# Kernel optimization log

Hardware: AMD Instinct MI355X
Metric: run time of the kernel (lower is better)

Reference implementation:

```python
import jax, jax.numpy as jnp
import numpy as np

D_MODEL = 256; N_HEADS = 8; N_LEVELS = 4; N_POINTS = 4; D_FFN = 1024
SHAPES = [(128, 128), (64, 64), (32, 32), (16, 16)]  # (H, W) per level, strides 8/16/32/64 of 1024x1024 input
B = 8; LQ = 1024
S_TOT = sum(h * w for h, w in SHAPES)


def setup_inputs() -> dict:
    key = jax.random.key(0)
    ks = iter(jax.random.split(key, 48))
    d = D_MODEL

    def f(shape, s=0.02):
        return jax.random.normal(next(ks), shape, dtype=jnp.float32) * s

    return {
        'tgt': f((B, LQ, d), 1.0),
        'query_pos': f((B, LQ, d), 1.0),
        'reference_points': jax.random.uniform(next(ks), (B, LQ, N_LEVELS, 2), dtype=jnp.float32),
        'src': f((B, S_TOT, d), 1.0),
        'w_in': f((3 * d, d)), 'b_in': jnp.zeros((3 * d,), jnp.float32),
        'w_out': f((d, d)), 'b_out': jnp.zeros((d,), jnp.float32),
        'ln1_g': jnp.ones((d,), jnp.float32), 'ln1_b': jnp.zeros((d,), jnp.float32),
        'ln2_g': jnp.ones((d,), jnp.float32), 'ln2_b': jnp.zeros((d,), jnp.float32),
        'ln3_g': jnp.ones((d,), jnp.float32), 'ln3_b': jnp.zeros((d,), jnp.float32),
        'w_val': f((d, d)), 'b_val': jnp.zeros((d,), jnp.float32),
        'w_off': f((N_HEADS * N_LEVELS * N_POINTS * 2, d), 0.002),
        'b_off': f((N_HEADS * N_LEVELS * N_POINTS * 2,), 0.5),
        'w_attw': f((N_HEADS * N_LEVELS * N_POINTS, d)),
        'b_attw': jnp.zeros((N_HEADS * N_LEVELS * N_POINTS,), jnp.float32),
        'w_oc': f((d, d)), 'b_oc': jnp.zeros((d,), jnp.float32),
        'w1': f((D_FFN, d)), 'b1': jnp.zeros((D_FFN,), jnp.float32),
        'w2': f((d, D_FFN)), 'b2': jnp.zeros((d,), jnp.float32),
        'spatial_shapes': jnp.array(SHAPES, dtype=jnp.int32),
    }


def layer_norm(x, g, b):
    mu = x.mean(-1, keepdims=True)
    var = ((x - mu) ** 2).mean(-1, keepdims=True)
    return (x - mu) * jax.lax.rsqrt(var + 1e-5) * g + b


def mha(tgt, query_pos, w_in, b_in, w_out, b_out):
    d = D_MODEL; Dh = d // N_HEADS
    Bs, Lq, _ = tgt.shape
    qk = tgt + query_pos
    q = (qk @ w_in[:d].T + b_in[:d]).reshape(Bs, Lq, N_HEADS, Dh)
    k = (qk @ w_in[d:2 * d].T + b_in[d:2 * d]).reshape(Bs, Lq, N_HEADS, Dh)
    v = (tgt @ w_in[2 * d:].T + b_in[2 * d:]).reshape(Bs, Lq, N_HEADS, Dh)
    attn = jax.nn.softmax(jnp.einsum('bqhd,bkhd->bhqk', q, k) / np.sqrt(Dh).astype(np.float32), axis=-1)
    o = jnp.einsum('bhqk,bkhd->bqhd', attn, v).reshape(Bs, Lq, d)
    return o @ w_out.T + b_out


def ms_deform_attn(value, loc, attw):
    # value [B,S,H,Dh]; loc [B,Lq,H,L,P,2] in [0,1]; attw [B,Lq,H,L,P]
    Bs, _, Hh, Dh = value.shape
    Lq = loc.shape[1]

    def to_hfirst(x):  # [B,Lq,Hh,P] -> [B,Hh,Lq*P,1]
        return jnp.transpose(x, (0, 2, 1, 3)).reshape(Bs, Hh, Lq * N_POINTS, 1)

    acc = jnp.zeros((Bs, Hh, Lq * N_POINTS, Dh), value.dtype)
    start = 0
    for l, (H_, W_) in enumerate(SHAPES):
        v = jnp.transpose(value[:, start:start + H_ * W_], (0, 2, 1, 3))  # [B,Hh,HW,Dh]
        start += H_ * W_
        ll = loc[:, :, :, l]  # [B,Lq,Hh,P,2]
        x = ll[..., 0] * W_ - 0.5
        y = ll[..., 1] * H_ - 0.5
        x0 = jnp.floor(x); y0 = jnp.floor(y)
        tx = x - x0; ty = y - y0

        def gather(xi, yi):
            valid = ((xi >= 0) & (xi < W_) & (yi >= 0) & (yi < H_)).astype(value.dtype)
            fi = (jnp.clip(yi, 0, H_ - 1) * W_ + jnp.clip(xi, 0, W_ - 1)).astype(jnp.int32)
            g = jnp.take_along_axis(v, to_hfirst(fi.astype(jnp.float32)).astype(jnp.int32), axis=2)
            return g * to_hfirst(valid)

        samp = (gather(x0, y0) * to_hfirst((1 - tx) * (1 - ty))
                + gather(x0 + 1, y0) * to_hfirst(tx * (1 - ty))
                + gather(x0, y0 + 1) * to_hfirst((1 - tx) * ty)
                + gather(x0 + 1, y0 + 1) * to_hfirst(tx * ty))
        acc = acc + samp * to_hfirst(attw[:, :, :, l])
    out = acc.reshape(Bs, Hh, Lq, N_POINTS, Dh).sum(3)  # [B,Hh,Lq,Dh]
    return jnp.transpose(out, (0, 2, 1, 3)).reshape(Bs, Lq, Hh * Dh)


def reference(tgt, query_pos, reference_points, src, w_in, b_in, w_out, b_out,
              ln1_g, ln1_b, ln2_g, ln2_b, ln3_g, ln3_b,
              w_val, b_val, w_off, b_off, w_attw, b_attw, w_oc, b_oc,
              w1, b1, w2, b2, spatial_shapes):
    Bs, Lq, d = tgt.shape
    Dh = d // N_HEADS
    # --- self attention (q=k=tgt+pos, v=tgt), residual + norm2 ---
    t2 = mha(tgt, query_pos, w_in, b_in, w_out, b_out)
    tgt = layer_norm(tgt + t2, ln2_g, ln2_b)
    # --- MSDeformAttn cross attention, residual + norm1 ---
    query = tgt + query_pos
    value = (src @ w_val.T + b_val).reshape(Bs, -1, N_HEADS, Dh)
    off = (query @ w_off.T + b_off).reshape(Bs, Lq, N_HEADS, N_LEVELS, N_POINTS, 2)
    aw = jax.nn.softmax((query @ w_attw.T + b_attw).reshape(Bs, Lq, N_HEADS, N_LEVELS * N_POINTS), axis=-1)
    aw = aw.reshape(Bs, Lq, N_HEADS, N_LEVELS, N_POINTS)
    normalizer = jnp.array([[w, h] for h, w in SHAPES], dtype=tgt.dtype)  # (W,H) per level
    loc = reference_points[:, :, None, :, None, :] + off / normalizer[None, None, None, :, None, :]
    ca = ms_deform_attn(value, loc, aw) @ w_oc.T + b_oc
    tgt = layer_norm(tgt + ca, ln1_g, ln1_b)
    # --- FFN, residual + norm3 ---
    t2 = jax.nn.relu(tgt @ w1.T + b1) @ w2.T + b2
    tgt = layer_norm(tgt + t2, ln3_g, ln3_b)
    return tgt
```

## Files before the change

### kernel.cpp

```cpp
#include <hip/hip_runtime.h>

typedef unsigned short ushort_t;
typedef unsigned int uint_t;
typedef __attribute__((ext_vector_type(8))) short short8;
typedef __attribute__((ext_vector_type(4))) float floatx4;
typedef __attribute__((ext_vector_type(4))) unsigned short ushortx4;

__device__ __forceinline__ ushort_t f2bf(float f){
  uint_t u = __builtin_bit_cast(uint_t, f);
  u += 0x7FFFu + ((u >> 16) & 1u);
  return (ushort_t)(u >> 16);
}
__device__ __forceinline__ float bf2f(ushort_t u){
  uint_t x = ((uint_t)u) << 16;
  return __builtin_bit_cast(float, x);
}
__device__ __forceinline__ uint_t packbf2(float a, float b){
  return (uint_t)f2bf(a) | ((uint_t)f2bf(b) << 16);
}

__device__ __forceinline__ void gload16(const void* g, void* l){
  __builtin_amdgcn_global_load_lds(
      (const __attribute__((address_space(1))) void*)g,
      (__attribute__((address_space(3))) void*)l, 16, 0, 0);
}

__global__ __launch_bounds__(256) void convert_w_kernel(const float* __restrict__ w_in_v,
    const float* __restrict__ w_val, const float* __restrict__ w_out,
    const float* __restrict__ w_oc, const float* __restrict__ w1,
    const float* __restrict__ w2, ushort_t* __restrict__ dst){
  int j = (blockIdx.x*256 + threadIdx.x) * 4;
  if (j >= 786432) return;
  const float* src; int off;
  if      (j <  65536){ src = w_in_v; off = 0;      }
  else if (j < 131072){ src = w_val;  off = 65536;  }
  else if (j < 196608){ src = w_out;  off = 131072; }
  else if (j < 262144){ src = w_oc;   off = 196608; }
  else if (j < 524288){ src = w1;     off = 262144; }
  else                { src = w2;     off = 524288; }
  float4 v = *(const float4*)(src + (j - off));
  uint2 u; u.x = packbf2(v.x, v.y); u.y = packbf2(v.z, v.w);
  *(uint2*)(dst + j) = u;
}

__global__ __launch_bounds__(256) void addln_kernel(const float* __restrict__ X,
    const float* __restrict__ Y, const float* __restrict__ gw,
    const float* __restrict__ bw, float* __restrict__ Out){
  int wave = threadIdx.x >> 6, lane = threadIdx.x & 63;
  long row = (long)blockIdx.x * 4 + wave;
  long base = row * 256 + lane * 4;
  float4 x = *(const float4*)(X + base);
  float4 y = *(const float4*)(Y + base);
  float v0=x.x+y.x, v1=x.y+y.y, v2=x.z+y.z, v3=x.w+y.w;
  float s  = v0+v1+v2+v3;
  float sq = v0*v0+v1*v1+v2*v2+v3*v3;
  #pragma unroll
  for (int off=32; off>0; off>>=1){
    s  += __shfl_xor(s, off);
    sq += __shfl_xor(sq, off);
  }
  float mu  = s * (1.f/256.f);
  float var = sq * (1.f/256.f) - mu*mu;
  float rs  = rsqrtf(var + 1e-5f);
  float4 g4 = *(const float4*)(gw + lane*4);
  float4 b4 = *(const float4*)(bw + lane*4);
  float4 o;
  o.x = (v0-mu)*rs*g4.x + b4.x;
  o.y = (v1-mu)*rs*g4.y + b4.y;
  o.z = (v2-mu)*rs*g4.z + b4.z;
  o.w = (v3-mu)*rs*g4.w + b4.w;
  *(float4*)(Out + base) = o;
}

__device__ __forceinline__ void stage_store(ushort_t* ls, int r, int c4, float4 v){
  int byte = r*64 + ((((c4>>1) ^ ((r>>1)&3)) << 4) | ((c4&1) << 3));
  uint2 u; u.x = packbf2(v.x, v.y); u.y = packbf2(v.z, v.w);
  *(uint2*)((char*)ls + byte) = u;
}
__device__ __forceinline__ short8 frag_load(const ushort_t* ls, int r, int g){
  int byte = r*64 + ((g ^ ((r>>1)&3)) << 4);
  return *(const short8*)((const char*)ls + byte);
}

__device__ __forceinline__ short8 frag_load_f32(const float* ls, int r, int g){
  const char* base = (const char*)ls + r*128;
  int x = r & 7;
  float4 f0 = *(const float4*)(base + ((((2*g)  ^ x)) << 4));
  float4 f1 = *(const float4*)(base + ((((2*g+1)^ x)) << 4));
  uint4 u;
  u.x = packbf2(f0.x, f0.y); u.y = packbf2(f0.z, f0.w);
  u.z = packbf2(f1.x, f1.y); u.w = packbf2(f1.z, f1.w);
  return __builtin_bit_cast(short8, u);
}

template<bool RELU, bool OUT_BF16>
__global__ __launch_bounds__(256) void gemm_dma_kernel(const float* __restrict__ A,
    const ushort_t* __restrict__ Wbf, const float* __restrict__ bias,
    void* __restrict__ Cout, int M, int N, int K){
  __shared__ float    ldsA[2][4096];
  __shared__ ushort_t ldsB[2][4096];
  const int t = threadIdx.x;
  const int lane = t & 63, wave = t >> 6;
  const int wm = wave >> 1, wn = wave & 1;
  const long rowA0 = (long)blockIdx.x * 128;
  const long rowB0 = (long)blockIdx.y * 128;
  const int rr = lane & 15, g = lane >> 4;
  const int arow  = lane >> 3;
  const int aslot = (lane & 7) ^ (arow & 7);
  const float* Abase = A + (rowA0 + wave*32 + arow)*(long)K + aslot*4;
  const int brow  = lane >> 2;
  const int bslot = lane & 3;
  floatx4 acc[4][4] = {};
  const int nsteps = K >> 5;

  #define ISSUE(kk, buf) do { \
    _Pragma("unroll") \
    for (int c=0;c<4;++c) \
      gload16(Abase + (kk) + (long)(8*c)*K, &ldsA[buf][(wave*32 + 8*c)*32]); \
    _Pragma("unroll") \
    for (int c=0;c<2;++c){ \
      int r_ = wave*32 + c*16 + brow; \
      const ushort_t* bs_ = Wbf + (rowB0 + r_)*(long)K + (kk) + (bslot ^ ((r_>>1)&3))*8; \
      gload16(bs_, (char*)ldsB[buf] + (wave*32 + c*16)*64); \
    } \
  } while(0)

  ISSUE(0, 0);
  if (nsteps > 1) ISSUE(32, 1);

  for (int k = 0; k < nsteps; ++k){
    if (k < nsteps-1) asm volatile("s_waitcnt vmcnt(6)" ::: "memory");
    else              asm volatile("s_waitcnt vmcnt(0)" ::: "memory");
    __builtin_amdgcn_s_barrier();
    const float*    lA = ldsA[k & 1];
    const ushort_t* lB = ldsB[k & 1];
    short8 af[4], bfr[4];
    #pragma unroll
    for (int mi=0;mi<4;++mi) af[mi]  = frag_load_f32(lA, wm*64 + mi*16 + rr, g);
    #pragma unroll
    for (int ni=0;ni<4;++ni) bfr[ni] = frag_load(lB, wn*64 + ni*16 + rr, g);
    #pragma unroll
    for (int mi=0;mi<4;++mi)
      #pragma unroll
      for (int ni=0;ni<4;++ni)
        acc[mi][ni] = __builtin_amdgcn_mfma_f32_16x16x32_bf16(af[mi], bfr[ni], acc[mi][ni], 0, 0, 0);
    __builtin_amdgcn_s_barrier();
    if (k + 2 < nsteps) ISSUE((k+2)*32, k & 1);
  }
  #undef ISSUE

  const int cg = lane >> 4;
  #pragma unroll
  for (int ni=0;ni<4;++ni){
    long n = rowB0 + wn*64 + ni*16 + (lane & 15);
    float bv = bias[n];
    #pragma unroll
    for (int mi=0;mi<4;++mi){
      long m = rowA0 + wm*64 + mi*16 + cg*4;
      #pragma unroll
      for (int r2=0;r2<4;++r2){
        float v = acc[mi][ni][r2] + bv;
        if (RELU) v = fmaxf(v, 0.f);
        if (OUT_BF16) ((ushort_t*)Cout)[(m+r2)*N + n] = f2bf(v);
        else          ((float*)Cout)[(m+r2)*N + n] = v;
      }
    }
  }
}

template<bool RELU, bool OUT_BF16>
__global__ __launch_bounds__(512, 4) void gemm_dma2_kernel(const float* __restrict__ A,
    const ushort_t* __restrict__ Wbf, const float* __restrict__ bias,
    void* __restrict__ Cout, int M, int N, int K){
  __shared__ float    ldsA[2][4096];
  __shared__ ushort_t ldsB[2][8192];
  const int t = threadIdx.x;
  const int lane = t & 63, wave = t >> 6;
  const int wm = wave >> 2, wn = wave & 3;
  const long rowA0 = (long)blockIdx.x * 128;
  const long n0 = (long)blockIdx.y * 256;
  const int rr = lane & 15, g = lane >> 4;
  const int arow_in = lane >> 3;
  const int aslot   = (lane & 7) ^ (arow_in & 7);
  const int brow_in = lane >> 2;
  const int bslot   = lane & 3;
  floatx4 acc[4][4] = {};
  const int nsteps = K >> 5;

  #define ISSUE2(kk, buf) do { \
    _Pragma("unroll") \
    for (int c=0;c<2;++c){ \
      int ar_ = (wave*2 + c)*8 + arow_in; \
      gload16(A + (rowA0 + ar_)*(long)K + (kk) + aslot*4, \
              &ldsA[buf][(wave*2 + c)*8*32]); \
    } \
    _Pragma("unroll") \
    for (int c=0;c<2;++c){ \
      int br_ = (wave*2 + c)*16 + brow_in; \
      const ushort_t* bs_ = Wbf + (n0 + br_)*(long)K + (kk) + (bslot ^ ((br_>>1)&3))*8; \
      gload16(bs_, (char*)ldsB[buf] + (wave*2 + c)*16*64); \
    } \
  } while(0)

  ISSUE2(0, 0);
  if (nsteps > 1) ISSUE2(32, 1);

  for (int k = 0; k < nsteps; ++k){
    if (k < nsteps-1) asm volatile("s_waitcnt vmcnt(4)" ::: "memory");
    else              asm volatile("s_waitcnt vmcnt(0)" ::: "memory");
    __builtin_amdgcn_s_barrier();
    const float*    lA = ldsA[k & 1];
    const ushort_t* lB = ldsB[k & 1];
    short8 af[4], bfr[4];
    #pragma unroll
    for (int mi=0;mi<4;++mi) af[mi]  = frag_load_f32(lA, wm*64 + mi*16 + rr, g);
    #pragma unroll
    for (int ni=0;ni<4;++ni) bfr[ni] = frag_load(lB, wn*64 + ni*16 + rr, g);
    #pragma unroll
    for (int mi=0;mi<4;++mi)
      #pragma unroll
      for (int ni=0;ni<4;++ni)
        acc[mi][ni] = __builtin_amdgcn_mfma_f32_16x16x32_bf16(af[mi], bfr[ni], acc[mi][ni], 0, 0, 0);
    __builtin_amdgcn_s_barrier();
    if (k + 2 < nsteps) ISSUE2((k+2)*32, k & 1);
  }
  #undef ISSUE2

  const int cg = lane >> 4;
  #pragma unroll
  for (int ni=0;ni<4;++ni){
    long n = n0 + wn*64 + ni*16 + (lane & 15);
    float bv = bias[n];
    #pragma unroll
    for (int mi=0;mi<4;++mi){
      long m = rowA0 + wm*64 + mi*16 + cg*4;
      #pragma unroll
      for (int r2=0;r2<4;++r2){
        float v = acc[mi][ni][r2] + bv;
        if (RELU) v = fmaxf(v, 0.f);
        if (OUT_BF16) ((ushort_t*)Cout)[(m+r2)*N + n] = f2bf(v);
        else          ((float*)Cout)[(m+r2)*N + n] = v;
      }
    }
  }
}

template<bool RELU>
__global__ __launch_bounds__(256) void gemm_add2_kernel(const float* __restrict__ A,
    const float* __restrict__ A2, const float* __restrict__ W,
    const float* __restrict__ bias, void* __restrict__ Cout,
    int M, int N, int K){
  __shared__ ushort_t lsA[4096], lsB[4096];
  const int t = threadIdx.x;
  const int lane = t & 63, wave = t >> 6;
  const int wm = wave >> 1, wn = wave & 1;
  const long rowA0 = (long)blockIdx.x * 128;
  const long rowB0 = (long)blockIdx.y * 128;
  floatx4 acc[4][4] = {};
  const int rr = lane & 15, g = lane >> 4;
  const int rA = t >> 3, c4 = t & 7;
  const float* Ap = A + (rowA0 + rA)*(long)K + c4*4;
  const float* A2p = A2 + (rowA0 + rA)*(long)K + c4*4;
  const float* Wp = W + (rowB0 + rA)*(long)K + c4*4;

  for (int k0 = 0; k0 < K; k0 += 32){
    __syncthreads();
    #pragma unroll
    for (int j=0;j<4;++j){
      float4 v = *(const float4*)(Ap + k0 + (long)(32*j)*K);
      float4 y = *(const float4*)(A2p + k0 + (long)(32*j)*K);
      v.x+=y.x; v.y+=y.y; v.z+=y.z; v.w+=y.w;
      stage_store(lsA, rA + 32*j, c4, v);
      stage_store(lsB, rA + 32*j, c4, *(const float4*)(Wp + k0 + (long)(32*j)*K));
    }
    __syncthreads();
    short8 af[4], bfr[4];
    #pragma unroll
    for (int mi=0;mi<4;++mi) af[mi]  = frag_load(lsA, wm*64 + mi*16 + rr, g);
    #pragma unroll
    for (int ni=0;ni<4;++ni) bfr[ni] = frag_load(lsB, wn*64 + ni*16 + rr, g);
    #pragma unroll
    for (int mi=0;mi<4;++mi)
      #pragma unroll
      for (int ni=0;ni<4;++ni)
        acc[mi][ni] = __builtin_amdgcn_mfma_f32_16x16x32_bf16(af[mi], bfr[ni], acc[mi][ni], 0, 0, 0);
  }
  const int cg = lane >> 4;
  #pragma unroll
  for (int ni=0;ni<4;++ni){
    long n = rowB0 + wn*64 + ni*16 + (lane & 15);
    float bv = bias[n];
    #pragma unroll
    for (int mi=0;mi<4;++mi){
      long m = rowA0 + wm*64 + mi*16 + cg*4;
      #pragma unroll
      for (int r2=0;r2<4;++r2){
        float v = acc[mi][ni][r2] + bv;
        if (RELU) v = fmaxf(v, 0.f);
        ((float*)Cout)[(m+r2)*N + n] = v;
      }
    }
  }
}

__global__ __launch_bounds__(256) void attn_mfma_kernel(const float* __restrict__ QK,
    const float* __restrict__ V, float* __restrict__ O){
  __shared__ ushort_t lsQ[4096];
  __shared__ ushort_t lsK[1024];
  __shared__ ushort_t lsVT[1024];
  __shared__ ushort_t lsP[4096];
  const int bh = blockIdx.y, b = bh >> 3, h = bh & 7;
  const int qt0 = blockIdx.x * 128;
  const int t = threadIdx.x, lane = t & 63, w = t >> 6;
  const int rr = lane & 15, g = lane >> 4;
  const float csc = 0.25506332f;

  const float* qbase = QK + ((long)b*1024 + qt0)*512 + h*32;
  #pragma unroll
  for (int j=0;j<4;++j){
    int i = t + j*256; int r = i>>3, c4i = i&7;
    float4 v = *(const float4*)(qbase + (long)r*512 + c4i*4);
    stage_store(lsQ, r, c4i, v);
  }
  __syncthreads();
  short8 bq[2];
  bq[0] = frag_load(lsQ, w*32 + rr, g);
  bq[1] = frag_load(lsQ, w*32 + 16 + rr, g);

  floatx4 accO[2][2] = {};
  float rsum[2] = {0.f, 0.f};
  const float* kbase = QK + (long)b*1024*512 + 256 + h*32;
  const float* vbase = V  + (long)b*1024*256 + h*32;

  for (int kt = 0; kt < 1024; kt += 32){
    __syncthreads();
    {
      int r = t >> 3, c4i = t & 7;
      float4 v = *(const float4*)(kbase + (long)(kt + r)*512 + c4i*4);
      stage_store(lsK, r, c4i, v);
    }
    {
      int kk = t >> 3, d4 = t & 7;
      float4 vv = *(const float4*)(vbase + (long)(kt + kk)*256 + d4*4);
      float vals[4] = {vv.x, vv.y, vv.z, vv.w};
      #pragma unroll
      for (int j=0;j<4;++j){
        int d = d4*4 + j;
        int cb = kk*2;
        int byte = d*64 + ((((cb>>4) ^ ((d>>1)&3)) << 4) | (cb & 15));
        *(ushort_t*)((char*)lsVT + byte) = f2bf(vals[j]);
      }
    }
    __syncthreads();
    floatx4 accS[2][2] = {};
    short8 ak0 = frag_load(lsK, rr, g);
    short8 ak1 = frag_load(lsK, 16 + rr, g);
    accS[0][0] = __builtin_amdgcn_mfma_f32_16x16x32_bf16(ak0, bq[0], accS[0][0], 0,0,0);
    accS[0][1] = __builtin_amdgcn_mfma_f32_16x16x32_bf16(ak0, bq[1], accS[0][1], 0,0,0);
    accS[1][0] = __builtin_amdgcn_mfma_f32_16x16x32_bf16(ak1, bq[0], accS[1][0], 0,0,0);
    accS[1][1] = __builtin_amdgcn_mfma_f32_16x16x32_bf16(ak1, bq[1], accS[1][1], 0,0,0);
    #pragma unroll
    for (int mi=0;mi<2;++mi){
      #pragma unroll
      for (int ni=0;ni<2;++ni){
        float p0 = exp2f(accS[mi][ni][0]*csc);
        float p1 = exp2f(accS[mi][ni][1]*csc);
        float p2 = exp2f(accS[mi][ni][2]*csc);
        float p3 = exp2f(accS[mi][ni][3]*csc);
        rsum[ni] += (p0+p1)+(p2+p3);
        int q   = w*32 + ni*16 + rr;
        int k0b = (mi*16 + g*4)*2;
        int byte = q*64 + ((((k0b>>4) ^ ((q>>1)&3)) << 4) | (k0b & 15));
        uint2 u; u.x = packbf2(p0,p1); u.y = packbf2(p2,p3);
        *(uint2*)((char*)lsP + byte) = u;
      }
    }
    short8 av0 = frag_load(lsVT, rr, g);
    short8 av1 = frag_load(lsVT, 16 + rr, g);
    short8 bp0 = frag_load(lsP, w*32 + rr, g);
    short8 bp1 = frag_load(lsP, w*32 + 16 + rr, g);
    accO[0][0] = __builtin_amdgcn_mfma_f32_16x16x32_bf16(av0, bp0, accO[0][0], 0,0,0);
    accO[0][1] = __builtin_amdgcn_mfma_f32_16x16x32_bf16(av0, bp1, accO[0][1], 0,0,0);
    accO[1][0] = __builtin_amdgcn_mfma_f32_16x16x32_bf16(av1, bp0, accO[1][0], 0,0,0);
    accO[1][1] = __builtin_amdgcn_mfma_f32_16x16x32_bf16(av1, bp1, accO[1][1], 0,0,0);
  }
  #pragma unroll
  for (int ni=0;ni<2;++ni){
    rsum[ni] += __shfl_xor(rsum[ni], 16);
    rsum[ni] += __shfl_xor(rsum[ni], 32);
    float inv = 1.f / rsum[ni];
    int q = qt0 + w*32 + ni*16 + rr;
    float* op = O + ((long)b*1024 + q)*256 + h*32;
    #pragma unroll
    for (int mi=0;mi<2;++mi){
      #pragma unroll
      for (int r2=0;r2<4;++r2){
        int d = mi*16 + g*4 + r2;
        op[d] = accO[mi][ni][r2] * inv;
      }
    }
  }
}

__global__ __launch_bounds__(256) void deform_kernel(const ushort_t* __restrict__ val,
    const float* __restrict__ offs, const float* __restrict__ awl,
    const float* __restrict__ refp, float* __restrict__ Out){
  __shared__ float s_off[1024], s_aw[512], s_ref[32];
  const int t = threadIdx.x;
  const long q0 = (long)blockIdx.x * 4;
  *(float4*)(s_off + t*4) = *(const float4*)(offs + q0*256 + t*4);
  if (t < 128) *(float4*)(s_aw + t*4) = *(const float4*)(awl + q0*128 + t*4);
  if (t < 32)  s_ref[t] = refp[q0*8 + t];
  __syncthreads();
  const int qi = t >> 6, tl = t & 63;
  const int h = tl >> 3, dq = (tl & 7) << 2;
  const int bq = (int)q0 + qi;
  const int b = bq >> 10;
  const float* offp = s_off + qi*256 + h*32;
  const float* awp  = s_aw  + qi*128 + h*16;
  const float* refq = s_ref + qi*8;
  float mx = -1e30f;
  #pragma unroll
  for (int i=0;i<16;++i) mx = fmaxf(mx, awp[i]);
  float p[16], sum = 0.f;
  #pragma unroll
  for (int i=0;i<16;++i){ p[i] = expf(awp[i]-mx); sum += p[i]; }
  float inv = 1.f/sum;
  const long vb = (long)b*21760*256 + h*32 + dq;
  const int Dim[4] = {128,64,32,16};
  const int St[4]  = {0,16384,20480,21504};
  float a0=0.f, a1=0.f, a2=0.f, a3=0.f;
  #pragma unroll
  for (int l=0;l<4;++l){
    const int Wl = Dim[l], Hl = Dim[l], st = St[l];
    float rx = refq[2*l], ry = refq[2*l+1];
    #pragma unroll
    for (int pp=0;pp<4;++pp){
      float x = rx*(float)Wl + offp[l*8+pp*2]   - 0.5f;
      float y = ry*(float)Hl + offp[l*8+pp*2+1] - 0.5f;
      float xf = floorf(x), yf = floorf(y);
      int x0 = (int)xf, y0 = (int)yf;
      float tx = x - xf, ty = y - yf;
      float s0=0.f,s1=0.f,s2=0.f,s3=0.f;
      #define CORNER(XI, YI, WGT) \
        if ((XI) >= 0 && (XI) < Wl && (YI) >= 0 && (YI) < Hl){ \
          ushortx4 u = *(const ushortx4*)(val + vb + (long)(st + (YI)*Wl + (XI))*256); \
          float wq = (WGT); \
          s0 += wq*bf2f(u[0]); s1 += wq*bf2f(u[1]); \
          s2 += wq*bf2f(u[2]); s3 += wq*bf2f(u[3]); \
        }
      CORNER(x0,   y0,   (1.f-tx)*(1.f-ty));
      CORNER(x0+1, y0,   tx*(1.f-ty));
      CORNER(x0,   y0+1, (1.f-tx)*ty);
      CORNER(x0+1, y0+1, tx*ty);
      #undef CORNER
      float pw = p[l*4+pp];
      a0 += pw*s0; a1 += pw*s1; a2 += pw*s2; a3 += pw*s3;
    }
  }
  float4 o; o.x=a0*inv; o.y=a1*inv; o.z=a2*inv; o.w=a3*inv;
  *(float4*)(Out + (long)bq*256 + h*32 + dq) = o;
}

extern "C" void kernel_launch(void* const* d_in, const int* in_sizes, int n_in,
                              void* d_out, int out_size, void* d_ws, size_t ws_size,
                              hipStream_t stream){
  (void)in_sizes; (void)n_in; (void)out_size; (void)ws_size;
  const float* tgt   = (const float*)d_in[0];
  const float* qpos  = (const float*)d_in[1];
  const float* refp  = (const float*)d_in[2];
  const float* src   = (const float*)d_in[3];
  const float* w_in  = (const float*)d_in[4];
  const float* b_in  = (const float*)d_in[5];
  const float* w_out = (const float*)d_in[6];
  const float* b_out = (const float*)d_in[7];
  const float* ln1g  = (const float*)d_in[8];
  const float* ln1b  = (const float*)d_in[9];
  const float* ln2g  = (const float*)d_in[10];
  const float* ln2b  = (const float*)d_in[11];
  const float* ln3g  = (const float*)d_in[12];
  const float* ln3b  = (const float*)d_in[13];
  const float* w_val = (const float*)d_in[14];
  const float* b_val = (const float*)d_in[15];
  const float* w_off = (const float*)d_in[16];
  const float* b_off = (const float*)d_in[17];
  const float* w_attw= (const float*)d_in[18];
  const float* b_attw= (const float*)d_in[19];
  const float* w_oc  = (const float*)d_in[20];
  const float* b_oc  = (const float*)d_in[21];
  const float* w1    = (const float*)d_in[22];
  const float* b1    = (const float*)d_in[23];
  const float* w2    = (const float*)d_in[24];
  const float* b2    = (const float*)d_in[25];

  float* ws = (float*)d_ws;
  float* bufQK  = ws + 2097152;
  float* bufOff = ws + 2097152;
  float* bufAW  = ws + 4194304;
  float* bufV   = ws + 6291456;
  float* bufO   = ws + 8388608;
  float* bufT2  = ws + 10485760;
  float* bufTg1 = ws + 12582912;
  float* bufTg2 = ws + 14680064;
  ushort_t* bufVal = (ushort_t*)(ws + 16777216);
  float* bufH   = ws + 16777216;
  ushort_t* bufWbf = (ushort_t*)(ws + 39059456);
  float* outF   = (float*)d_out;

  const ushort_t* winvbf = bufWbf;
  const ushort_t* wvalbf = bufWbf + 65536;
  const ushort_t* woutbf = bufWbf + 131072;
  const ushort_t* wocbf  = bufWbf + 196608;
  const ushort_t* w1bf   = bufWbf + 262144;
  const ushort_t* w2bf   = bufWbf + 524288;

  dim3 B256(256), B512(512);
  convert_w_kernel<<<dim3(768), B256, 0, stream>>>(w_in + 512*256, w_val, w_out, w_oc, w1, w2, bufWbf);
  gemm_add2_kernel<false><<<dim3(64,4), B256, 0, stream>>>(tgt, qpos, w_in, b_in, bufQK, 8192, 512, 256);
  gemm_dma_kernel<false,false><<<dim3(64,2), B256, 0, stream>>>(tgt, winvbf, b_in + 512, bufV, 8192, 256, 256);
  attn_mfma_kernel<<<dim3(8,64), B256, 0, stream>>>(bufQK, bufV, bufO);
  gemm_dma_kernel<false,false><<<dim3(64,2), B256, 0, stream>>>(bufO, woutbf, b_out, bufT2, 8192, 256, 256);
  addln_kernel<<<dim3(2048), B256, 0, stream>>>(tgt, bufT2, ln2g, ln2b, bufTg1);
  gemm_dma2_kernel<false,true><<<dim3(1360,1), B512, 0, stream>>>(src, wvalbf, b_val, bufVal, 174080, 256, 256);
  gemm_add2_kernel<false><<<dim3(64,2), B256, 0, stream>>>(bufTg1, qpos, w_off, b_off, bufOff, 8192, 256, 256);
  gemm_add2_kernel<false><<<dim3(64,1), B256, 0, stream>>>(bufTg1, qpos, w_attw, b_attw, bufAW, 8192, 128, 256);
  deform_kernel<<<dim3(2048), B256, 0, stream>>>(bufVal, bufOff, bufAW, refp, bufO);
  gemm_dma_kernel<false,false><<<dim3(64,2), B256, 0, stream>>>(bufO, wocbf, b_oc, bufT2, 8192, 256, 256);
  addln_kernel<<<dim3(2048), B256, 0, stream>>>(bufTg1, bufT2, ln1g, ln1b, bufTg2);
  gemm_dma2_kernel<true,false><<<dim3(64,4), B512, 0, stream>>>(bufTg2, w1bf, b1, bufH, 8192, 1024, 256);
  gemm_dma_kernel<false,false><<<dim3(64,2), B256, 0, stream>>>(bufH, w2bf, b2, bufT2, 8192, 256, 1024);
  addln_kernel<<<dim3(2048), B256, 0, stream>>>(bufTg2, bufT2, ln3g, ln3b, outF);
}
```

Baseline: 350.2 us.

## Fuse offset and attention-weight projections, branchless deform sampling, wider FFN2 GEMM

Packs w_off/w_attw and their biases into one weight matrix so a single GEMM produces both sampling offsets and attention logits, with the deform kernel reading the concatenated layout. This drops one launch and a second pass over the input activations. Bilinear corner loads become branchless: indices are clamped and out-of-range weights zeroed, which removes divergence but issues loads for corners that were previously skipped. The second FFN GEMM switches to the 512-thread dma2 kernel with one column block, which changes its tiling and occupancy.

```diff
diff --git a/kernel.cpp b/kernel.cpp
--- a/kernel.cpp
+++ b/kernel.cpp
@@ -41,6 +41,19 @@
   float4 v = *(const float4*)(src + (j - off));
   uint2 u; u.x = packbf2(v.x, v.y); u.y = packbf2(v.z, v.w);
   *(uint2*)(dst + j) = u;
+}
+
+__global__ __launch_bounds__(256) void pack_offattw_kernel(const float* __restrict__ w_off,
+    const float* __restrict__ w_attw, const float* __restrict__ b_off,
+    const float* __restrict__ b_attw, float* __restrict__ dst){
+  int j = (blockIdx.x*256 + threadIdx.x) * 4;
+  if (j >= 98688) return;
+  const float* src; int off;
+  if      (j < 65536){ src = w_off;  off = 0;     }
+  else if (j < 98304){ src = w_attw; off = 65536; }
+  else if (j < 98560){ src = b_off;  off = 98304; }
+  else               { src = b_attw; off = 98560; }
+  *(float4*)(dst + j) = *(const float4*)(src + (j - off));
 }
 
 __global__ __launch_bounds__(256) void addln_kernel(const float* __restrict__ X,
@@ -403,21 +416,22 @@
 }
 
 __global__ __launch_bounds__(256) void deform_kernel(const ushort_t* __restrict__ val,
-    const float* __restrict__ offs, const float* __restrict__ awl,
-    const float* __restrict__ refp, float* __restrict__ Out){
-  __shared__ float s_off[1024], s_aw[512], s_ref[32];
+    const float* __restrict__ offaw, const float* __restrict__ refp,
+    float* __restrict__ Out){
+  __shared__ float s_cat[1536], s_ref[32];
   const int t = threadIdx.x;
   const long q0 = (long)blockIdx.x * 4;
-  *(float4*)(s_off + t*4) = *(const float4*)(offs + q0*256 + t*4);
-  if (t < 128) *(float4*)(s_aw + t*4) = *(const float4*)(awl + q0*128 + t*4);
+  const float* srcOA = offaw + q0*384;
+  *(float4*)(s_cat + t*4) = *(const float4*)(srcOA + t*4);
+  if (t < 128) *(float4*)(s_cat + 1024 + t*4) = *(const float4*)(srcOA + 1024 + t*4);
   if (t < 32)  s_ref[t] = refp[q0*8 + t];
   __syncthreads();
   const int qi = t >> 6, tl = t & 63;
   const int h = tl >> 3, dq = (tl & 7) << 2;
   const int bq = (int)q0 + qi;
   const int b = bq >> 10;
-  const float* offp = s_off + qi*256 + h*32;
-  const float* awp  = s_aw  + qi*128 + h*16;
+  const float* offp = s_cat + qi*384 + h*32;
+  const float* awp  = s_cat + qi*384 + 256 + h*16;
   const float* refq = s_ref + qi*8;
   float mx = -1e30f;
   #pragma unroll
@@ -442,13 +456,15 @@
       int x0 = (int)xf, y0 = (int)yf;
       float tx = x - xf, ty = y - yf;
       float s0=0.f,s1=0.f,s2=0.f,s3=0.f;
-      #define CORNER(XI, YI, WGT) \
-        if ((XI) >= 0 && (XI) < Wl && (YI) >= 0 && (YI) < Hl){ \
-          ushortx4 u = *(const ushortx4*)(val + vb + (long)(st + (YI)*Wl + (XI))*256); \
-          float wq = (WGT); \
-          s0 += wq*bf2f(u[0]); s1 += wq*bf2f(u[1]); \
-          s2 += wq*bf2f(u[2]); s3 += wq*bf2f(u[3]); \
-        }
+      #define CORNER(XI, YI, WGT) { \
+        int xi_ = (XI), yi_ = (YI); \
+        bool valid_ = (xi_ >= 0) & (xi_ < Wl) & (yi_ >= 0) & (yi_ < Hl); \
+        int xc_ = min(max(xi_, 0), Wl-1), yc_ = min(max(yi_, 0), Hl-1); \
+        ushortx4 u = *(const ushortx4*)(val + vb + (long)(st + yc_*Wl + xc_)*256); \
+        float wq = valid_ ? (WGT) : 0.f; \
+        s0 += wq*bf2f(u[0]); s1 += wq*bf2f(u[1]); \
+        s2 += wq*bf2f(u[2]); s3 += wq*bf2f(u[3]); \
+      }
       CORNER(x0,   y0,   (1.f-tx)*(1.f-ty));
       CORNER(x0+1, y0,   tx*(1.f-ty));
       CORNER(x0,   y0+1, (1.f-tx)*ty);
@@ -495,8 +511,7 @@
 
   float* ws = (float*)d_ws;
   float* bufQK  = ws + 2097152;
-  float* bufOff = ws + 2097152;
-  float* bufAW  = ws + 4194304;
+  float* bufOA  = ws + 2097152;
   float* bufV   = ws + 6291456;
   float* bufO   = ws + 8388608;
   float* bufT2  = ws + 10485760;
@@ -505,6 +520,7 @@
   ushort_t* bufVal = (ushort_t*)(ws + 16777216);
   float* bufH   = ws + 16777216;
   ushort_t* bufWbf = (ushort_t*)(ws + 39059456);
+  float* bufWOA = ws + 39452672;
   float* outF   = (float*)d_out;
 
   const ushort_t* winvbf = bufWbf;
@@ -516,18 +532,18 @@
 
   dim3 B256(256), B512(512);
   convert_w_kernel<<<dim3(768), B256, 0, stream>>>(w_in + 512*256, w_val, w_out, w_oc, w1, w2, bufWbf);
+  pack_offattw_kernel<<<dim3(97), B256, 0, stream>>>(w_off, w_attw, b_off, b_attw, bufWOA);
   gemm_add2_kernel<false><<<dim3(64,4), B256, 0, stream>>>(tgt, qpos, w_in, b_in, bufQK, 8192, 512, 256);
   gemm_dma_kernel<false,false><<<dim3(64,2), B256, 0, stream>>>(tgt, winvbf, b_in + 512, bufV, 8192, 256, 256);
   attn_mfma_kernel<<<dim3(8,64), B256, 0, stream>>>(bufQK, bufV, bufO);
   gemm_dma_kernel<false,false><<<dim3(64,2), B256, 0, stream>>>(bufO, woutbf, b_out, bufT2, 8192, 256, 256);
   addln_kernel<<<dim3(2048), B256, 0, stream>>>(tgt, bufT2, ln2g, ln2b, bufTg1);
   gemm_dma2_kernel<false,true><<<dim3(1360,1), B512, 0, stream>>>(src, wvalbf, b_val, bufVal, 174080, 256, 256);
-  gemm_add2_kernel<false><<<dim3(64,2), B256, 0, stream>>>(bufTg1, qpos, w_off, b_off, bufOff, 8192, 256, 256);
-  gemm_add2_kernel<false><<<dim3(64,1), B256, 0, stream>>>(bufTg1, qpos, w_attw, b_attw, bufAW, 8192, 128, 256);
-  deform_kernel<<<dim3(2048), B256, 0, stream>>>(bufVal, bufOff, bufAW, refp, bufO);
+  gemm_add2_kernel<false><<<dim3(64,3), B256, 0, stream>>>(bufTg1, qpos, bufWOA, bufWOA + 98304, bufOA, 8192, 384, 256);
+  deform_kernel<<<dim3(2048), B256, 0, stream>>>(bufVal, bufOA, refp, bufO);
   gemm_dma_kernel<false,false><<<dim3(64,2), B256, 0, stream>>>(bufO, wocbf, b_oc, bufT2, 8192, 256, 256);
   addln_kernel<<<dim3(2048), B256, 0, stream>>>(bufTg1, bufT2, ln1g, ln1b, bufTg2);
   gemm_dma2_kernel<true,false><<<dim3(64,4), B512, 0, stream>>>(bufTg2, w1bf, b1, bufH, 8192, 1024, 256);
-  gemm_dma_kernel<false,false><<<dim3(64,2), B256, 0, stream>>>(bufH, w2bf, b2, bufT2, 8192, 256, 1024);
+  gemm_dma2_kernel<false,false><<<dim3(64,1), B512, 0, stream>>>(bufH, w2bf, b2, bufT2, 8192, 256, 1024);
   addln_kernel<<<dim3(2048), B256, 0, stream>>>(bufTg2, bufT2, ln3g, ln3b, outF);
 }
```

Measured after the change: 317.6 us. 9.3% less time.
